# Performance work log

Hardware: AMD Instinct MI355X
Metric: run time of the kernel (lower is better)

## Reference

```python
import jax, jax.numpy as jnp
import numpy as np

HIDDEN = 2048
HEADS = 16
HEAD_DIM = HIDDEN // HEADS
D_FF = 4 * HIDDEN
B, T = 2, 2048
LN_EPS = 1e-5


def setup_inputs() -> dict:
    key = jax.random.key(0)
    ks = jax.random.split(key, 12)
    s = 0.02
    x = jax.random.normal(ks[0], (B, T, HIDDEN), dtype=jnp.float32)
    # strict upper-triangular True == masked (causal)
    causal_mask = jnp.triu(jnp.ones((T, T), dtype=bool), k=1)
    # weights stored as [in, out] (equivalent to torch Linear weight.T)
    Wq = jax.random.normal(ks[1], (HIDDEN, HIDDEN), jnp.float32) * s
    Wk = jax.random.normal(ks[2], (HIDDEN, HIDDEN), jnp.float32) * s
    Wv = jax.random.normal(ks[3], (HIDDEN, HIDDEN), jnp.float32) * s
    Wo = jax.random.normal(ks[4], (HIDDEN, HIDDEN), jnp.float32) * s
    ln1_w = jnp.ones((HIDDEN,), jnp.float32)
    ln1_b = jnp.zeros((HIDDEN,), jnp.float32)
    ln2_w = jnp.ones((HIDDEN,), jnp.float32)
    ln2_b = jnp.zeros((HIDDEN,), jnp.float32)
    W1 = jax.random.normal(ks[5], (HIDDEN, D_FF), jnp.float32) * s
    b1 = jnp.zeros((D_FF,), jnp.float32)
    W2 = jax.random.normal(ks[6], (D_FF, HIDDEN), jnp.float32) * s
    b2 = jnp.zeros((HIDDEN,), jnp.float32)
    return dict(x=x, causal_mask=causal_mask, Wq=Wq, Wk=Wk, Wv=Wv, Wo=Wo,
                ln1_w=ln1_w, ln1_b=ln1_b, ln2_w=ln2_w, ln2_b=ln2_b,
                W1=W1, b1=b1, W2=W2, b2=b2)


def _layernorm(x, w, b):
    mu = jnp.mean(x, axis=-1, keepdims=True)
    var = jnp.mean(jnp.square(x - mu), axis=-1, keepdims=True)
    return (x - mu) * jax.lax.rsqrt(var + LN_EPS) * w + b


def reference(x, causal_mask, Wq, Wk, Wv, Wo, ln1_w, ln1_b, ln2_w, ln2_b, W1, b1, W2, b2):
    Bx, Tx, H = x.shape
    h = _layernorm(x, ln1_w, ln1_b)
    # [B, T, heads, head_dim] -> [B, heads, T, head_dim]
    q = (h @ Wq).reshape(Bx, Tx, HEADS, HEAD_DIM).transpose(0, 2, 1, 3)
    k = (h @ Wk).reshape(Bx, Tx, HEADS, HEAD_DIM).transpose(0, 2, 1, 3)
    v = (h @ Wv).reshape(Bx, Tx, HEADS, HEAD_DIM).transpose(0, 2, 1, 3)
    scale = 1.0 / jnp.sqrt(jnp.float32(HEAD_DIM))
    scores = jnp.einsum('bhqd,bhkd->bhqk', q, k) * scale  # [B, heads, T, T]
    scores = jnp.where(causal_mask, -jnp.inf, scores)
    attn = jax.nn.softmax(scores, axis=-1)
    out = jnp.einsum('bhqk,bhkd->bhqd', attn, v)  # [B, heads, T, head_dim]
    out = out.transpose(0, 2, 1, 3).reshape(Bx, Tx, H)
    x = x + out @ Wo
    h2 = _layernorm(x, ln2_w, ln2_b)
    mlp = jax.nn.silu(h2 @ W1 + b1) @ W2 + b2
    return x + mlp
```

## Files before the change

### kernel.cpp

```cpp
#include <hip/hip_runtime.h>

#define HID 2048
#define NH 16
#define DH 128
#define DFF 8192
#define BB 2
#define TT 2048
#define MROWS 4096

typedef __bf16 bf16x8 __attribute__((ext_vector_type(8)));
typedef __bf16 bf16x4 __attribute__((ext_vector_type(4)));
typedef float  f32x4  __attribute__((ext_vector_type(4)));

__device__ __forceinline__ f32x4 mfma16(bf16x8 a, bf16x8 b, f32x4 c) {
    return __builtin_amdgcn_mfma_f32_16x16x32_bf16(a, b, c, 0, 0, 0);
}

__device__ __forceinline__ void gload_lds16(const __bf16* gsrc, __bf16* ldst) {
    __builtin_amdgcn_global_load_lds(
        (const __attribute__((address_space(1))) void*)gsrc,
        (__attribute__((address_space(3))) void*)ldst, 16, 0, 0);
}

template<int K, int N>
__global__ __launch_bounds__(256) void transpose_bf16_kernel(
    const float* __restrict__ W, __bf16* __restrict__ Wt) {
    __shared__ float tile[64][65];
    int tx = threadIdx.x;
    int ty = threadIdx.y;
    int n0 = blockIdx.x * 64;
    int k0 = blockIdx.y * 64;
    #pragma unroll
    for (int i = 0; i < 16; i++) {
        int kk = ty * 16 + i;
        tile[tx][kk] = W[(size_t)(k0 + kk) * N + n0 + tx];
    }
    __syncthreads();
    #pragma unroll
    for (int i = 0; i < 16; i++) {
        int nn = ty * 16 + i;
        Wt[(size_t)(n0 + nn) * K + k0 + tx] = (__bf16)tile[nn][tx];
    }
}

__global__ __launch_bounds__(256) void ln_kernel(
    const float* __restrict__ x, const float* __restrict__ gw,
    const float* __restrict__ gb, __bf16* __restrict__ out) {
    int row = blockIdx.x;
    int t = threadIdx.x;
    const float* xr = x + (size_t)row * HID;
    float4 v0 = *(const float4*)(xr + t * 8);
    float4 v1 = *(const float4*)(xr + t * 8 + 4);
    float xv[8] = {v0.x, v0.y, v0.z, v0.w, v1.x, v1.y, v1.z, v1.w};
    float s = 0.f, q = 0.f;
    #pragma unroll
    for (int j = 0; j < 8; j++) { s += xv[j]; q += xv[j] * xv[j]; }
    #pragma unroll
    for (int off = 1; off < 64; off <<= 1) {
        s += __shfl_xor(s, off);
        q += __shfl_xor(q, off);
    }
    __shared__ float ssum[4], ssq[4];
    if ((t & 63) == 0) { ssum[t >> 6] = s; ssq[t >> 6] = q; }
    __syncthreads();
    s = ssum[0] + ssum[1] + ssum[2] + ssum[3];
    q = ssq[0] + ssq[1] + ssq[2] + ssq[3];
    float mu = s * (1.0f / HID);
    float var = q * (1.0f / HID) - mu * mu;
    float rs = rsqrtf(var + 1e-5f);
    bf16x8 o;
    #pragma unroll
    for (int j = 0; j < 8; j++)
        o[j] = (__bf16)((xv[j] - mu) * rs * gw[t * 8 + j] + gb[t * 8 + j]);
    *(bf16x8*)(out + (size_t)row * HID + t * 8) = o;
}

template<int HB>
__global__ __launch_bounds__(256) void init_resid_kernel(
    const float* __restrict__ src, const float* __restrict__ bias,
    float* __restrict__ out) {
    int i = blockIdx.x * 256 + threadIdx.x;
    float4 a = ((const float4*)src)[i];
    if constexpr (HB) {
        float4 bb = ((const float4*)bias)[i & (HID / 4 - 1)];
        a.x += bb.x; a.y += bb.y; a.z += bb.z; a.w += bb.w;
    }
    ((float4*)out)[i] = a;
}

template<int EPI, int KSPLIT, int N, int K>
__global__ __launch_bounds__(512, 1) void gemm256(
    const __bf16* __restrict__ A, const __bf16* __restrict__ Bt,
    void* __restrict__ C0, void* __restrict__ C1, void* __restrict__ C2,
    const float* __restrict__ resid, const float* __restrict__ bias, int nN) {
    constexpr int BK = 64;
    constexpr int KS = K / KSPLIT;
    constexpr int NT = KS / BK;

    __shared__ __align__(16) __bf16 As[2][16384];
    __shared__ __align__(16) __bf16 Bs[2][16384];

    int tid = threadIdx.x;
    int w = tid >> 6, l = tid & 63;
    int wm = w >> 2, wn = w & 3;
    int qi = l & 15, g = l >> 4;

    int nwg = gridDim.x;
    int bid = blockIdx.x;
    int wg = (bid & 7) * (nwg >> 3) + (bid >> 3);
    int nMN = nwg / KSPLIT;
    int tileid = wg % nMN;
    int kh = wg / nMN;
    int bm = tileid / nN, bn = tileid % nN;
    int row0 = bm * 256, col0 = bn * 256;
    int kb0 = kh * KS;

    int offA[2][2], offB[2][2];
    #pragma unroll
    for (int h = 0; h < 2; h++)
        #pragma unroll
        for (int i = 0; i < 2; i++) {
            int slot = i * 512 + tid;
            int r = slot >> 3, u8 = slot & 7;
            offA[h][i] = (row0 + h * 128 + r) * K + kb0 + (u8 ^ (r & 7)) * 8;
            offB[h][i] = (col0 + h * 128 + r) * K + kb0 + (u8 ^ (r & 7)) * 8;
        }
    int dstoff = w * 512;

    int xk0 = (g * 16) ^ ((qi & 7) << 4);
    int xk1 = (64 + g * 16) ^ ((qi & 7) << 4);
    int aoff = wm * 8192 + qi * 128;
    int boff = wn * 4096 + qi * 128;

    f32x4 acc[8][4] = {};
    bf16x8 aF[4][2], bF0[2][2], bF1[2][2];

    auto stageA = [&](int u, int h) {
        #pragma unroll
        for (int i = 0; i < 2; i++)
            gload_lds16(A + offA[h][i] + u * BK,
                        &As[u & 1][h * 8192 + i * 4096 + dstoff]);
    };
    auto stageB = [&](int u, int h) {
        #pragma unroll
        for (int i = 0; i < 2; i++)
            gload_lds16(Bt + offB[h][i] + u * BK,
                        &Bs[u & 1][h * 8192 + i * 4096 + dstoff]);
    };
    auto loadA = [&](int s, int qm) {
        const char* pa0 = (const char*)As[s] + aoff + xk0;
        const char* pa1 = (const char*)As[s] + aoff + xk1;
        #pragma unroll
        for (int mi = 0; mi < 4; mi++) {
            aF[mi][0] = *(const bf16x8*)(pa0 + qm * 16384 + mi * 2048);
            aF[mi][1] = *(const bf16x8*)(pa1 + qm * 16384 + mi * 2048);
        }
    };
    auto loadB = [&](bf16x8 (&bF)[2][2], int s, int qn) {
        const char* pb0 = (const char*)Bs[s] + boff + xk0;
        const char* pb1 = (const char*)Bs[s] + boff + xk1;
        #pragma unroll
        for (int ni = 0; ni < 2; ni++) {
            bF[ni][0] = *(const bf16x8*)(pb0 + qn * 16384 + ni * 2048);
            bF[ni][1] = *(const bf16x8*)(pb1 + qn * 16384 + ni * 2048);
        }
    };

    #define MMAC(BF, FMB, FNB)                                             \
        asm volatile("s_waitcnt lgkmcnt(0)" ::: "memory");                 \
        __builtin_amdgcn_sched_barrier(0);                                 \
        __builtin_amdgcn_s_setprio(1);                                     \
        _Pragma("unroll")                                                  \
        for (int kk = 0; kk < 2; kk++)                                     \
            _Pragma("unroll")                                              \
            for (int mi = 0; mi < 4; mi++)                                 \
                _Pragma("unroll")                                          \
                for (int ni = 0; ni < 2; ni++)                             \
                    acc[(FMB) + mi][(FNB) + ni] =                          \
                        mfma16(aF[mi][kk], BF[ni][kk],                     \
                               acc[(FMB) + mi][(FNB) + ni]);               \
        __builtin_amdgcn_s_setprio(0);

    stageA(0, 0); stageB(0, 0); stageA(0, 1); stageB(0, 1);
    if (NT > 1) { stageA(1, 0); stageB(1, 0); stageA(1, 1); }
    asm volatile("s_waitcnt vmcnt(6)" ::: "memory");
    __builtin_amdgcn_s_barrier();

    for (int t = 0; t < NT; t++) {
        int s = t & 1;
        loadA(s, 0); loadB(bF0, s, 0);
        if (t + 1 < NT) stageB(t + 1, 1);
        __builtin_amdgcn_s_barrier();
        MMAC(bF0, 0, 0)
        __builtin_amdgcn_s_barrier();
        loadB(bF1, s, 1);
        if (t + 2 < NT) stageA(t + 2, 0);
        __builtin_amdgcn_s_barrier();
        MMAC(bF1, 0, 2)
        __builtin_amdgcn_s_barrier();
        loadA(s, 1);
        if (t + 2 < NT) stageB(t + 2, 0);
        __builtin_amdgcn_s_barrier();
        MMAC(bF0, 4, 0)
        __builtin_amdgcn_s_barrier();
        if (t + 2 < NT) stageA(t + 2, 1);
        __builtin_amdgcn_s_barrier();
        MMAC(bF1, 4, 2)
        if (t + 2 < NT)      asm volatile("s_waitcnt vmcnt(6)" ::: "memory");
        else if (t + 1 < NT) asm volatile("s_waitcnt vmcnt(0)" ::: "memory");
        __builtin_amdgcn_s_barrier();
    }
    #undef MMAC

    #pragma unroll
    for (int fm = 0; fm < 8; fm++) {
        int qm = fm >> 2, mi = fm & 3;
        int Rb = row0 + qm * 128 + wm * 64 + mi * 16 + g * 4;
        #pragma unroll
        for (int fn = 0; fn < 4; fn++) {
            int qn = fn >> 1, ni = fn & 1;
            int C = col0 + qn * 128 + wn * 32 + ni * 16 + qi;
            f32x4 v = acc[fm][fn];
            if constexpr (EPI == 6) {
                int region = C >> 11;
                int Cl = C & 2047;
                if (region < 2) {
                    __bf16* dst = (__bf16*)(region == 0 ? C0 : C1);
                    #pragma unroll
                    for (int r = 0; r < 4; r++)
                        dst[(size_t)(Rb + r) * 2048 + Cl] = (__bf16)v[r];
                } else {
                    bf16x4 pk;
                    #pragma unroll
                    for (int r = 0; r < 4; r++) pk[r] = (__bf16)v[r];
                    int b = Rb >> 11, t0 = Rb & 2047, hh = Cl >> 7, d = Cl & 127;
                    *(bf16x4*)((__bf16*)C2 +
                        ((size_t)(b * NH + hh) * DH + d) * TT + t0) = pk;
                }
            } else {
                #pragma unroll
                for (int r = 0; r < 4; r++) {
                    size_t idx = (size_t)(Rb + r) * N + C;
                    if constexpr (EPI == 2) {
                        ((float*)C0)[idx] = resid[idx] + v[r];
                    } else if constexpr (EPI == 3) {
                        float u = v[r] + bias[C];
                        ((__bf16*)C0)[idx] = (__bf16)(u / (1.f + __expf(-u)));
                    } else if constexpr (EPI == 5) {
                        atomicAdd((float*)C0 + idx, v[r]);
                    }
                }
            }
        }
    }
}

__global__ __launch_bounds__(256) void attn_kernel(
    const __bf16* __restrict__ qh, const __bf16* __restrict__ kh,
    const __bf16* __restrict__ vt, __bf16* __restrict__ out) {
    __shared__ __align__(16) __bf16 Ks[64 * 128];
    __shared__ __align__(16) __bf16 Vts[128 * 64];
    __shared__ __align__(16) __bf16 plds[4][1024];
    int tid = threadIdx.x;
    int w = tid >> 6, l = tid & 63;
    int qi = l & 15, g = l >> 4;
    int bh = blockIdx.y;
    int b = bh >> 4, hd = bh & 15;
    int qtile = gridDim.x - 1 - blockIdx.x;
    int qbase = qtile * 64 + w * 16;
    int qg = qbase + qi;

    const __bf16* qrow = qh + ((size_t)b * TT + qg) * HID + hd * DH;
    const __bf16* kbase = kh + (size_t)b * TT * HID + hd * DH;
    const __bf16* vtb = vt + (size_t)bh * DH * TT;

    bf16x8 bq[4];
    #pragma unroll
    for (int kc = 0; kc < 4; kc++)
        bq[kc] = *(const bf16x8*)(qrow + kc * 32 + g * 8);

    f32x4 O[8] = {};
    float m_run = -3.0e38f, l_run = 0.f;
    const float scale = 0.08838834764831845f;
    int nt = qtile + 1;

    for (int it = 0; it < nt; it++) {
        int kv0 = it * 64;
        __syncthreads();
        #pragma unroll
        for (int i = 0; i < 4; i++) {
            int j = (w * 4 + i) * 64 + l;
            int r = j >> 4, u = j & 15;
            int cb = (u * 16) ^ ((r & 7) << 4);
            gload_lds16(kbase + (size_t)(kv0 + r) * HID + (cb >> 1),
                        Ks + (w * 4 + i) * 512);
        }
        #pragma unroll
        for (int i = 0; i < 4; i++) {
            int j = (w * 4 + i) * 64 + l;
            int r = j >> 3, u = j & 7;
            int cb = (u * 16) ^ ((r & 7) << 4);
            gload_lds16(vtb + (size_t)r * TT + kv0 + (cb >> 1),
                        Vts + (w * 4 + i) * 512);
        }
        __syncthreads();

        f32x4 st[4] = {};
        #pragma unroll
        for (int t = 0; t < 4; t++) {
            #pragma unroll
            for (int kc = 0; kc < 4; kc++) {
                int row = t * 16 + qi;
                int cb = (kc * 64 + g * 16) ^ ((qi & 7) << 4);
                bf16x8 ak = *(const bf16x8*)(Ks + row * 128 + (cb >> 1));
                st[t] = mfma16(ak, bq[kc], st[t]);
            }
        }
        float s[16];
        #pragma unroll
        for (int t = 0; t < 4; t++)
            #pragma unroll
            for (int r = 0; r < 4; r++) s[t * 4 + r] = st[t][r] * scale;
        #pragma unroll
        for (int i = 0; i < 16; i++) {
            int kvg = kv0 + (i >> 2) * 16 + g * 4 + (i & 3);
            if (kvg > qg) s[i] = -3.0e38f;
        }
        float mt = s[0];
        #pragma unroll
        for (int i = 1; i < 16; i++) mt = fmaxf(mt, s[i]);
        mt = fmaxf(mt, __shfl_xor(mt, 16));
        mt = fmaxf(mt, __shfl_xor(mt, 32));
        float m_new = fmaxf(m_run, mt);
        float alpha = __expf(m_run - m_new);
        float p[16], ps = 0.f;
        #pragma unroll
        for (int i = 0; i < 16; i++) { p[i] = __expf(s[i] - m_new); ps += p[i]; }
        ps += __shfl_xor(ps, 16);
        ps += __shfl_xor(ps, 32);
        l_run = l_run * alpha + ps;
        m_run = m_new;

        #pragma unroll
        for (int t = 0; t < 4; t++) {
            bf16x4 pk;
            #pragma unroll
            for (int r = 0; r < 4; r++) pk[r] = (__bf16)p[t * 4 + r];
            int cb = (t * 32 + g * 8) ^ ((qi & 7) << 4);
            *(bf16x4*)(&plds[w][qi * 64 + (cb >> 1)]) = pk;
        }

        float av[4];
        #pragma unroll
        for (int r = 0; r < 4; r++) av[r] = __shfl(alpha, (g << 4) | (g * 4 + r));
        #pragma unroll
        for (int oc = 0; oc < 8; oc++)
            #pragma unroll
            for (int r = 0; r < 4; r++) O[oc][r] *= av[r];

        #pragma unroll
        for (int h = 0; h < 2; h++) {
            int cbp = (h * 64 + g * 16) ^ ((qi & 7) << 4);
            bf16x8 ap = *(const bf16x8*)(&plds[w][qi * 64 + (cbp >> 1)]);
            #pragma unroll
            for (int oc = 0; oc < 8; oc++) {
                int row = oc * 16 + qi;
                int cb = (h * 64 + g * 16) ^ ((qi & 7) << 4);
                bf16x8 bv = *(const bf16x8*)(Vts + row * 64 + (cb >> 1));
                O[oc] = mfma16(ap, bv, O[oc]);
            }
        }
    }

    float linv[4];
    #pragma unroll
    for (int r = 0; r < 4; r++) {
        float lq = __shfl(l_run, (g << 4) | (g * 4 + r));
        linv[r] = 1.0f / lq;
    }
    __bf16* op = out + ((size_t)b * TT + qbase) * HID + hd * DH;
    #pragma unroll
    for (int oc = 0; oc < 8; oc++)
        #pragma unroll
        for (int r = 0; r < 4; r++)
            op[(size_t)(g * 4 + r) * HID + oc * 16 + qi] = (__bf16)(O[oc][r] * linv[r]);
}

extern "C" void kernel_launch(void* const* d_in, const int* in_sizes, int n_in,
                              void* d_out, int out_size, void* d_ws, size_t ws_size,
                              hipStream_t stream) {
    const float* x    = (const float*)d_in[0];
    const float* Wq   = (const float*)d_in[2];
    const float* Wk   = (const float*)d_in[3];
    const float* Wv   = (const float*)d_in[4];
    const float* Wo   = (const float*)d_in[5];
    const float* ln1w = (const float*)d_in[6];
    const float* ln1b = (const float*)d_in[7];
    const float* ln2w = (const float*)d_in[8];
    const float* ln2b = (const float*)d_in[9];
    const float* W1   = (const float*)d_in[10];
    const float* b1   = (const float*)d_in[11];
    const float* W2   = (const float*)d_in[12];
    const float* b2   = (const float*)d_in[13];
    float* outp = (float*)d_out;

    char* ws = (char*)d_ws;
    const size_t SZ_W   = (size_t)HID * HID * 2;
    const size_t SZ_WF  = (size_t)HID * DFF * 2;
    const size_t SZ_ACT = (size_t)MROWS * HID * 2;
    const size_t SZ_X32 = (size_t)MROWS * HID * 4;

    __bf16* wqT  = (__bf16*)(ws);
    __bf16* wkT  = (__bf16*)(ws + SZ_W);
    __bf16* wvT  = (__bf16*)(ws + 2 * SZ_W);
    __bf16* woT  = (__bf16*)(ws + 3 * SZ_W);
    __bf16* w1T  = (__bf16*)(ws + 4 * SZ_W);
    __bf16* w2T  = (__bf16*)(ws + 4 * SZ_W + SZ_WF);
    __bf16* h    = (__bf16*)(ws + 4 * SZ_W + 2 * SZ_WF);
    float*  x1   = (float*) (ws + 4 * SZ_W + 2 * SZ_WF + SZ_ACT);
    char*   base = ws + 4 * SZ_W + 2 * SZ_WF + SZ_ACT + SZ_X32;
    __bf16* qb   = (__bf16*)(base);
    __bf16* kb   = (__bf16*)(base + SZ_ACT);
    __bf16* vtb  = (__bf16*)(base + 2 * SZ_ACT);
    __bf16* attn = (__bf16*)(base + 3 * SZ_ACT);
    __bf16* mlp1 = (__bf16*)(base);

    dim3 blk256(256), blk512(512);
    transpose_bf16_kernel<HID, HID><<<dim3(32, 32), dim3(64, 4), 0, stream>>>(Wq, wqT);
    transpose_bf16_kernel<HID, HID><<<dim3(32, 32), dim3(64, 4), 0, stream>>>(Wk, wkT);
    transpose_bf16_kernel<HID, HID><<<dim3(32, 32), dim3(64, 4), 0, stream>>>(Wv, wvT);
    transpose_bf16_kernel<HID, HID><<<dim3(32, 32), dim3(64, 4), 0, stream>>>(Wo, woT);
    transpose_bf16_kernel<HID, DFF><<<dim3(128, 32), dim3(64, 4), 0, stream>>>(W1, w1T);
    transpose_bf16_kernel<DFF, HID><<<dim3(32, 128), dim3(64, 4), 0, stream>>>(W2, w2T);

    ln_kernel<<<MROWS, blk256, 0, stream>>>(x, ln1w, ln1b, h);

    gemm256<6, 1, 6144, HID><<<384, blk512, 0, stream>>>(
        h, wqT, qb, kb, vtb, nullptr, nullptr, 24);

    attn_kernel<<<dim3(TT / 64, BB * NH), blk256, 0, stream>>>(qb, kb, vtb, attn);

    init_resid_kernel<0><<<MROWS * HID / 4 / 256, blk256, 0, stream>>>(x, nullptr, x1);
    gemm256<5, 2, HID, HID><<<256, blk512, 0, stream>>>(
        attn, woT, x1, nullptr, nullptr, nullptr, nullptr, 8);

    ln_kernel<<<MROWS, blk256, 0, stream>>>(x1, ln2w, ln2b, h);

    gemm256<3, 1, DFF, HID><<<512, blk512, 0, stream>>>(
        h, w1T, mlp1, nullptr, nullptr, nullptr, b1, 32);

    init_resid_kernel<1><<<MROWS * HID / 4 / 256, blk256, 0, stream>>>(x1, b2, outp);
    gemm256<5, 2, HID, DFF><<<256, blk512, 0, stream>>>(
        mlp1, w2T, outp, nullptr, nullptr, nullptr, nullptr, 8);
}
```

Before: 793.1 us.

## Restructure GEMM main loop to prefetch LDS fragments across iterations

Reorders the GEMM K-loop schedule so that LDS fragment loads for the next quadrant and next tile are issued before the current MFMA block, using partial lgkmcnt waits instead of full drains. It drops several barriers per iteration and shifts the staging of global-to-LDS copies and the vmcnt thresholds. The aim is to overlap LDS reads and global loads with MFMA work. The new ordering carries a risk of LDS hazards if the waitcnt counts or barrier placement are wrong.

```diff
diff --git a/kernel.cpp b/kernel.cpp
--- a/kernel.cpp
+++ b/kernel.cpp
@@ -166,9 +166,7 @@
         }
     };
 
-    #define MMAC(BF, FMB, FNB)                                             \
-        asm volatile("s_waitcnt lgkmcnt(0)" ::: "memory");                 \
-        __builtin_amdgcn_sched_barrier(0);                                 \
+    #define MMAC_Q(BF, FMB, FNB)                                           \
         __builtin_amdgcn_s_setprio(1);                                     \
         _Pragma("unroll")                                                  \
         for (int kk = 0; kk < 2; kk++)                                     \
@@ -182,35 +180,43 @@
         __builtin_amdgcn_s_setprio(0);
 
     stageA(0, 0); stageB(0, 0); stageA(0, 1); stageB(0, 1);
-    if (NT > 1) { stageA(1, 0); stageB(1, 0); stageA(1, 1); }
-    asm volatile("s_waitcnt vmcnt(6)" ::: "memory");
+    if (NT > 1) { stageA(1, 0); stageB(1, 0); }
+    if (NT > 1) asm volatile("s_waitcnt vmcnt(4)" ::: "memory");
+    else        asm volatile("s_waitcnt vmcnt(0)" ::: "memory");
     __builtin_amdgcn_s_barrier();
+    loadA(0, 0);
+    loadB(bF0, 0, 0);
 
     for (int t = 0; t < NT; t++) {
         int s = t & 1;
-        loadA(s, 0); loadB(bF0, s, 0);
+        __builtin_amdgcn_s_barrier();
+        if (t + 1 < NT) stageA(t + 1, 1);
+        loadB(bF1, s, 1);
+        asm volatile("s_waitcnt lgkmcnt(4)" ::: "memory");
+        __builtin_amdgcn_sched_barrier(0);
+        MMAC_Q(bF0, 0, 0)
+        __builtin_amdgcn_s_barrier();
         if (t + 1 < NT) stageB(t + 1, 1);
+        asm volatile("s_waitcnt lgkmcnt(0)" ::: "memory");
+        __builtin_amdgcn_sched_barrier(0);
+        MMAC_Q(bF1, 0, 2)
+        loadA(s, 1);
         __builtin_amdgcn_s_barrier();
-        MMAC(bF0, 0, 0)
-        __builtin_amdgcn_s_barrier();
-        loadB(bF1, s, 1);
         if (t + 2 < NT) stageA(t + 2, 0);
-        __builtin_amdgcn_s_barrier();
-        MMAC(bF1, 0, 2)
-        __builtin_amdgcn_s_barrier();
-        loadA(s, 1);
-        if (t + 2 < NT) stageB(t + 2, 0);
-        __builtin_amdgcn_s_barrier();
-        MMAC(bF0, 4, 0)
-        __builtin_amdgcn_s_barrier();
-        if (t + 2 < NT) stageA(t + 2, 1);
-        __builtin_amdgcn_s_barrier();
-        MMAC(bF1, 4, 2)
-        if (t + 2 < NT)      asm volatile("s_waitcnt vmcnt(6)" ::: "memory");
+        asm volatile("s_waitcnt lgkmcnt(0)" ::: "memory");
+        __builtin_amdgcn_sched_barrier(0);
+        MMAC_Q(bF0, 4, 0)
+        if (t + 2 < NT)      asm volatile("s_waitcnt vmcnt(2)" ::: "memory");
         else if (t + 1 < NT) asm volatile("s_waitcnt vmcnt(0)" ::: "memory");
         __builtin_amdgcn_s_barrier();
-    }
-    #undef MMAC
+        if (t + 2 < NT) stageB(t + 2, 0);
+        MMAC_Q(bF1, 4, 2)
+        if (t + 1 < NT) {
+            loadA(s ^ 1, 0);
+            loadB(bF0, s ^ 1, 0);
+        }
+    }
+    #undef MMAC_Q
 
     #pragma unroll
     for (int fm = 0; fm < 8; fm++) {
```

Measured after the change: 797.3 us. Within noise of the previous version (+0.5%).
